# Performance work log

Hardware: AMD Instinct MI355X
Metric: run time of the kernel (lower is better)

## Reference

```python
import jax, jax.numpy as jnp
import numpy as np

INPUT_DIM = 29
OUTPUT_DIM = 67
ES = 256
HS = 512
SRC_LEN = 64
TRG_LEN = 48
BATCH = 512


def _lstm_cell(x, h, c, Wih, Whh, bih, bhh):
    # PyTorch gate order: i, f, g, o
    g = x @ Wih.T + bih + h @ Whh.T + bhh
    i, f, gg, o = jnp.split(g, 4, axis=-1)
    c_new = jax.nn.sigmoid(f) * c + jax.nn.sigmoid(i) * jnp.tanh(gg)
    h_new = jax.nn.sigmoid(o) * jnp.tanh(c_new)
    return h_new, c_new


def setup_inputs() -> dict:
    key = jax.random.key(0)
    ks = jax.random.split(key, 32)
    s_es = 1.0 / np.sqrt(ES)
    s_hs = 1.0 / np.sqrt(HS)
    inp = {}
    inp['src'] = jax.random.randint(ks[0], (SRC_LEN, BATCH), 0, INPUT_DIM)
    inp['trg'] = jax.random.randint(ks[1], (TRG_LEN, BATCH), 0, OUTPUT_DIM)
    # encoder params
    inp['enc_emb'] = jax.random.normal(ks[2], (INPUT_DIM, ES), jnp.float32)
    inp['enc_Wih_f'] = jax.random.normal(ks[3], (4 * HS, ES), jnp.float32) * s_hs
    inp['enc_Whh_f'] = jax.random.normal(ks[4], (4 * HS, HS), jnp.float32) * s_hs
    inp['enc_bih_f'] = jax.random.normal(ks[5], (4 * HS,), jnp.float32) * s_hs
    inp['enc_bhh_f'] = jax.random.normal(ks[6], (4 * HS,), jnp.float32) * s_hs
    inp['enc_Wih_b'] = jax.random.normal(ks[7], (4 * HS, ES), jnp.float32) * s_hs
    inp['enc_Whh_b'] = jax.random.normal(ks[8], (4 * HS, HS), jnp.float32) * s_hs
    inp['enc_bih_b'] = jax.random.normal(ks[9], (4 * HS,), jnp.float32) * s_hs
    inp['enc_bhh_b'] = jax.random.normal(ks[10], (4 * HS,), jnp.float32) * s_hs
    inp['fc_h_W'] = jax.random.normal(ks[11], (HS, 2 * HS), jnp.float32) * s_hs
    inp['fc_h_b'] = jax.random.normal(ks[12], (HS,), jnp.float32) * s_hs
    inp['fc_c_W'] = jax.random.normal(ks[13], (HS, 2 * HS), jnp.float32) * s_hs
    inp['fc_c_b'] = jax.random.normal(ks[14], (HS,), jnp.float32) * s_hs
    # decoder params
    inp['dec_emb'] = jax.random.normal(ks[15], (OUTPUT_DIM, ES), jnp.float32)
    inp['dec_Wih'] = jax.random.normal(ks[16], (4 * HS, 2 * HS + ES), jnp.float32) * s_hs
    inp['dec_Whh'] = jax.random.normal(ks[17], (4 * HS, HS), jnp.float32) * s_hs
    inp['dec_bih'] = jax.random.normal(ks[18], (4 * HS,), jnp.float32) * s_hs
    inp['dec_bhh'] = jax.random.normal(ks[19], (4 * HS,), jnp.float32) * s_hs
    inp['energy_W'] = jax.random.normal(ks[20], (1, 3 * HS), jnp.float32) * s_hs
    inp['energy_b'] = jax.random.normal(ks[21], (1,), jnp.float32) * s_hs
    inp['fc_out_W'] = jax.random.normal(ks[22], (OUTPUT_DIM, HS), jnp.float32) * s_hs
    inp['fc_out_b'] = jax.random.normal(ks[23], (OUTPUT_DIM,), jnp.float32) * s_hs
    return inp


def _forward(src, trg, enc_emb, enc_Wih_f, enc_Whh_f, enc_bih_f, enc_bhh_f,
             enc_Wih_b, enc_Whh_b, enc_bih_b, enc_bhh_b,
             fc_h_W, fc_h_b, fc_c_W, fc_c_b,
             dec_emb, dec_Wih, dec_Whh, dec_bih, dec_bhh,
             energy_W, energy_b, fc_out_W, fc_out_b):
    S, B = src.shape
    T = trg.shape[0]
    emb = enc_emb[src]  # [S, B, ES]
    h0 = jnp.zeros((B, HS), emb.dtype)
    c0 = jnp.zeros((B, HS), emb.dtype)

    def fwd_step(carry, x_t):
        h, c = carry
        h, c = _lstm_cell(x_t, h, c, enc_Wih_f, enc_Whh_f, enc_bih_f, enc_bhh_f)
        return (h, c), h

    def bwd_step(carry, x_t):
        h, c = carry
        h, c = _lstm_cell(x_t, h, c, enc_Wih_b, enc_Whh_b, enc_bih_b, enc_bhh_b)
        return (h, c), h

    (hf, cf), out_f = jax.lax.scan(fwd_step, (h0, c0), emb)
    (hb, cb), out_b_rev = jax.lax.scan(bwd_step, (h0, c0), emb[::-1])
    out_b = out_b_rev[::-1]
    encoder_states = jnp.concatenate([out_f, out_b], axis=2)  # [S, B, 2H]

    # fc_h / fc_c compress the 2 directions' final hidden/cell to [B, H]
    hidden_h = jnp.concatenate([hf, hb], axis=-1) @ fc_h_W.T + fc_h_b
    hidden_c = jnp.concatenate([cf, cb], axis=-1) @ fc_c_W.T + fc_c_b

    # Attention: original code passes encoder_hidden on EVERY step, so the
    # attention weights and context vector are constant across decode steps.
    h_rep = jnp.broadcast_to(hidden_h[None], (S, B, HS))
    e_in = jnp.concatenate([h_rep, encoder_states], axis=2)  # [S, B, 3H]
    energy = jax.nn.relu(e_in @ energy_W.T + energy_b)  # [S, B, 1]
    attn = jax.nn.softmax(energy, axis=0)[..., 0]  # [S, B]
    context = jnp.einsum('sb,sbh->bh', attn, encoder_states)  # [B, 2H]

    # Decode: teacher_forcing_ratio = 1.0 -> inputs are trg[t-1]; since the
    # rnn initial state is reset to encoder_hidden each step, all T-1 steps
    # are independent and can be computed in parallel.
    dec_in_tok = trg[:-1]  # [T-1, B]
    emb_d = dec_emb[dec_in_tok]  # [T-1, B, ES]
    ctx_rep = jnp.broadcast_to(context[None], (T - 1, B, 2 * HS))
    rnn_in = jnp.concatenate([ctx_rep, emb_d], axis=2)  # [T-1, B, 2H+ES]
    h_new, _ = _lstm_cell(rnn_in, hidden_h[None], hidden_c[None],
                          dec_Wih, dec_Whh, dec_bih, dec_bhh)
    logits = h_new @ fc_out_W.T + fc_out_b  # [T-1, B, V]
    outputs = jnp.concatenate(
        [jnp.zeros((1, B, OUTPUT_DIM), logits.dtype), logits], axis=0)
    return outputs


def reference(src, trg, enc_emb, enc_Wih_f, enc_Whh_f, enc_bih_f, enc_bhh_f,
              enc_Wih_b, enc_Whh_b, enc_bih_b, enc_bhh_b,
              fc_h_W, fc_h_b, fc_c_W, fc_c_b,
              dec_emb, dec_Wih, dec_Whh, dec_bih, dec_bhh,
              energy_W, energy_b, fc_out_W, fc_out_b):
    return _forward(src, trg, enc_emb, enc_Wih_f, enc_Whh_f, enc_bih_f,
                    enc_bhh_f, enc_Wih_b, enc_Whh_b, enc_bih_b, enc_bhh_b,
                    fc_h_W, fc_h_b, fc_c_W, fc_c_b, dec_emb, dec_Wih,
                    dec_Whh, dec_bih, dec_bhh, energy_W, energy_b,
                    fc_out_W, fc_out_b)
```

## Files before the change

kernel.cpp:

```cpp
#include <hip/hip_runtime.h>
#include <cstddef>

#define BATCH 512
#define ESZ   256
#define HSZ   512
#define G4    2048
#define SRCL  64
#define TRGL  48
#define ODIM  67

typedef __bf16  bf8v    __attribute__((ext_vector_type(8)));
typedef __bf16  bf4v    __attribute__((ext_vector_type(4)));
typedef float   floatx4 __attribute__((ext_vector_type(4)));

__device__ __forceinline__ floatx4 MF(bf8v a, bf8v b, floatx4 c) {
    return __builtin_amdgcn_mfma_f32_16x16x32_bf16(a, b, c, 0, 0, 0);
}

__device__ __forceinline__ float frcp(float x) { return __builtin_amdgcn_rcpf(x); }
__device__ __forceinline__ float fsig(float x) { return frcp(1.0f + __expf(-x)); }
__device__ __forceinline__ float ftanh(float x) { return 1.0f - 2.0f * frcp(1.0f + __expf(2.0f * x)); }

__device__ __forceinline__ bf8v cvt8(const float* __restrict__ s) {
    float4 a = *(const float4*)s;
    float4 b = *(const float4*)(s + 4);
    bf8v v;
    v[0] = (__bf16)a.x; v[1] = (__bf16)a.y; v[2] = (__bf16)a.z; v[3] = (__bf16)a.w;
    v[4] = (__bf16)b.x; v[5] = (__bf16)b.y; v[6] = (__bf16)b.z; v[7] = (__bf16)b.w;
    return v;
}

__global__ void embed_swz(const int* __restrict__ tok, const float* __restrict__ table,
                          __bf16* __restrict__ Az) {
    int i = blockIdx.x * 256 + threadIdx.x;
    int lane = i & 63;
    int kt = (i >> 6) & 7;
    int mt = (i >> 9) & 31;
    int t  = i >> 14;
    int b = mt * 16 + (lane & 15);
    int k = kt * 32 + (lane >> 4) * 8;
    int tk = tok[t * BATCH + b];
    (void)kt;
    *(bf8v*)(Az + (size_t)i * 8) = cvt8(table + (size_t)tk * ESZ + k);
}

__global__ void embdz(const int* __restrict__ trg, const float* __restrict__ table,
                      __bf16* __restrict__ Dz) {
    int i = blockIdx.x * 256 + threadIdx.x;
    int lane = i & 63;
    int kt = (i >> 6) & 7;
    int mt = i >> 9;
    int row = mt * 16 + (lane & 15);
    int k = kt * 32 + (lane >> 4) * 8;
    int tk = trg[row];
    *(bf8v*)(Dz + (size_t)i * 8) = cvt8(table + (size_t)tk * ESZ + k);
}

__global__ void zero_kernel(float* __restrict__ p, int n) {
    int i = blockIdx.x * 256 + threadIdx.x;
    if (i < n) p[i] = 0.f;
}

__global__ void bias_prep(const float* __restrict__ af, const float* __restrict__ bf,
                          const float* __restrict__ ab, const float* __restrict__ bb,
                          const float* __restrict__ ad, const float* __restrict__ bd,
                          float* __restrict__ of, float* __restrict__ ob, float* __restrict__ od) {
    int i = blockIdx.x * 256 + threadIdx.x;
    if (i < G4) { of[i] = af[i] + bf[i]; ob[i] = ab[i] + bb[i]; od[i] = ad[i] + bd[i]; }
}

__global__ void wswz_bf16(const float* __restrict__ Wih, const float* __restrict__ Whh,
                          __bf16* __restrict__ Wz) {
    int i = blockIdx.x * 256 + threadIdx.x;
    int lane = i & 63;
    int rest = i >> 6;
    int kt = rest % 24;
    int gj = rest / 24;
    int g = gj & 3, jt = gj >> 2;
    int row = g * 512 + jt * 16 + (lane & 15);
    int k = kt * 32 + (lane >> 4) * 8;
    const float* src = (k < ESZ) ? (Wih + (size_t)row * ESZ + k)
                                 : (Whh + (size_t)row * HSZ + (k - ESZ));
    *(bf8v*)(Wz + (size_t)i * 8) = cvt8(src);
}

__global__ void decwz(const float* __restrict__ dec_Wih, __bf16* __restrict__ Wz) {
    int i = blockIdx.x * 256 + threadIdx.x;
    int lane = i & 63;
    int kt = (i >> 6) & 7;
    int nt = i >> 9;
    int row = nt * 16 + (lane & 15);
    int k = kt * 32 + (lane >> 4) * 8;
    *(bf8v*)(Wz + (size_t)i * 8) =
        cvt8(dec_Wih + (size_t)row * (2 * HSZ + ESZ) + 2 * HSZ + k);
}

__global__ void wdcat_bf16(const float* __restrict__ dec_Wih, const float* __restrict__ dec_Whh,
                           __bf16* __restrict__ Wd) {
    int i = blockIdx.x * 256 + threadIdx.x;
    int n = i / 192;
    int e = (i - n * 192) << 3;
    const float* src = (e < 1024) ? (dec_Wih + (size_t)n * 1280 + e)
                                  : (dec_Whh + (size_t)n * HSZ + (e - 1024));
    *(bf8v*)(Wd + (size_t)n * 1536 + e) = cvt8(src);
}

__global__ void conv_f2b(const float* __restrict__ src, __bf16* __restrict__ dst, int n8) {
    int i = blockIdx.x * 256 + threadIdx.x;
    if (i < n8) *(bf8v*)(dst + (size_t)i * 8) = cvt8(src + (size_t)i * 8);
}

__global__ void fo_pad(const float* __restrict__ W, __bf16* __restrict__ dst) {
    int i = blockIdx.x * 256 + threadIdx.x;
    int r = i >> 6, e = (i & 63) << 3;
    bf8v v;
    if (r < ODIM) v = cvt8(W + (size_t)r * HSZ + e);
    else { for (int k = 0; k < 8; ++k) v[k] = (__bf16)0.f; }
    *(bf8v*)(dst + (size_t)r * HSZ + e) = v;
}

__global__ void fragswz(const __bf16* __restrict__ src, __bf16* __restrict__ dst,
                        int KT, int nchunks) {
    int i = blockIdx.x * 256 + threadIdx.x;
    if (i >= nchunks) return;
    int lane = i & 63;
    int kt = (i >> 6) % KT;
    int nt = (i >> 6) / KT;
    int row = nt * 16 + (lane & 15);
    int k = kt * 32 + (lane >> 4) * 8;
    *(bf8v*)(dst + (size_t)i * 8) = *(const bf8v*)(src + (size_t)row * (KT * 32) + k);
}

__global__ void cat_hfb(const __bf16* __restrict__ es, __bf16* __restrict__ dst) {
    int i = blockIdx.x * 256 + threadIdx.x;
    int r = i >> 7, e = (i & 127) << 3;
    const __bf16* s = (e < HSZ) ? (es + ((size_t)(63 * BATCH + r)) * 1024 + e)
                                : (es + (size_t)r * 1024 + e);
    *(bf8v*)(dst + (size_t)r * 1024 + e) = *(const bf8v*)s;
}

__global__ void cat_cfb(const float* __restrict__ cbuf, __bf16* __restrict__ dst) {
    int i = blockIdx.x * 256 + threadIdx.x;
    int r = i >> 7, e = (i & 127) << 3;
    const float* s = (e < HSZ) ? (cbuf + (size_t)r * HSZ + e)
                               : (cbuf + (size_t)BATCH * HSZ + (size_t)r * HSZ + (e - HSZ));
    *(bf8v*)(dst + (size_t)r * 1024 + e) = cvt8(s);
}

__global__ void cat_ctxh(const float* __restrict__ ctx, const float* __restrict__ hid_h,
                         __bf16* __restrict__ dst) {
    int i = blockIdx.x * 256 + threadIdx.x;
    int r = i / 192;
    int e = (i - r * 192) << 3;
    const float* s = (e < 1024) ? (ctx + (size_t)r * 1024 + e)
                                : (hid_h + (size_t)r * HSZ + (e - 1024));
    *(bf8v*)(dst + (size_t)r * 1536 + e) = cvt8(s);
}

__global__ void d0_swz(const float* __restrict__ D0, float* __restrict__ D0s) {
    int i = blockIdx.x * 256 + threadIdx.x;
    int b = i >> 11, rest = i & 2047, g = rest >> 9, j = rest & 511;
    D0s[(((size_t)b * 512 + j) << 2) + g] = D0[i];
}

__global__ __launch_bounds__(256) void enc_step6(
    const __bf16* __restrict__ Az, const __bf16* __restrict__ hPrev,
    __bf16* __restrict__ hNext, float* __restrict__ cbuf, __bf16* __restrict__ es,
    const __bf16* __restrict__ WzF, const __bf16* __restrict__ WzB,
    const float* __restrict__ biasF, const float* __restrict__ biasB, int t)
{
    __shared__ __bf16 Bh[4 * 16 * 64 * 8];
    __shared__ float  hT[64 * 17];

    const int dir = blockIdx.z;
    const int tt  = dir ? (SRCL - 1 - t) : t;
    const __bf16* Wz  = dir ? WzB : WzF;
    const float* bias = dir ? biasB : biasF;
    const int jt = blockIdx.x;
    const int j0 = jt * 16;
    const int m0 = blockIdx.y * 64;

    const int tid = threadIdx.x;
    const int w = tid >> 6, lane = tid & 63;
    const int quad = lane >> 4, l15 = lane & 15;

    const __bf16* WzJ = Wz + (((size_t)jt * 4 * 24) << 9);

#pragma unroll
    for (int it = 0; it < 16; ++it) {
        int idx = tid + it * 256;
        *(bf8v*)(Bh + ((size_t)idx << 3)) =
            *(const bf8v*)(WzJ + (((size_t)(((idx >> 10) * 24 + 8 + ((idx >> 6) & 15)) * 64
                                            + (idx & 63))) << 3));
    }

    const int mt = (m0 >> 4) + w;
    floatx4 acc[4] = {};

    const __bf16* ax = Az + ((((size_t)tt * 32 + mt) * 8) << 9) + lane * 8;
#pragma unroll
    for (int kt = 0; kt < 8; ++kt) {
        bf8v a = *(const bf8v*)(ax + ((size_t)kt << 9));
#pragma unroll
        for (int g = 0; g < 4; ++g) {
            bf8v b = *(const bf8v*)(WzJ + (((size_t)((g * 24 + kt) * 64 + lane)) << 3));
            acc[g] = MF(a, b, acc[g]);
        }
    }
    __syncthreads();
    const __bf16* ah = hPrev + ((((size_t)dir * 32 + mt) * 16) << 9) + lane * 8;
#pragma unroll 4
    for (int kt = 0; kt < 16; ++kt) {
        bf8v a = *(const bf8v*)(ah + ((size_t)kt << 9));
#pragma unroll
        for (int g = 0; g < 4; ++g) {
            bf8v b = *(const bf8v*)(Bh + (((size_t)((g * 16 + kt) * 64 + lane)) << 3));
            acc[g] = MF(a, b, acc[g]);
        }
    }

    const int j = j0 + l15;
    const float b0 = bias[j], b1 = bias[HSZ + j], b2 = bias[2 * HSZ + j], b3 = bias[3 * HSZ + j];
    const size_t cb = (size_t)dir * BATCH * HSZ;
    const int mwb = w * 16 + quad * 4;
#pragma unroll
    for (int r = 0; r < 4; ++r) {
        int m = m0 + mwb + r;
        float gi = acc[0][r] + b0;
        float gf = acc[1][r] + b1;
        float gg = acc[2][r] + b2;
        float go = acc[3][r] + b3;
        size_t ci = cb + (size_t)m * HSZ + j;
        float cn = fsig(gf) * cbuf[ci] + fsig(gi) * ftanh(gg);
        cbuf[ci] = cn;
        hT[(mwb + r) * 17 + l15] = fsig(go) * ftanh(cn);
    }
    __syncthreads();

    {
        int r = tid >> 2, ch = tid & 3;
        const float* hp = &hT[r * 17 + ch * 4];
        bf4v v;
#pragma unroll
        for (int e = 0; e < 4; ++e) v[e] = (__bf16)hp[e];
        *(bf4v*)(es + ((size_t)tt * BATCH + m0 + r) * 1024 + dir * HSZ + j0 + ch * 4) = v;
    }
    if (tid < 128) {
        int mtl = tid >> 5;
        int lnsub = tid & 31;
        int jhalf = (j0 >> 4) & 1;
        int ln = lnsub + jhalf * 32;
        int mloc = mtl * 16 + (lnsub & 15);
        int jloc = (lnsub >> 4) * 8;
        const float* hp = &hT[mloc * 17 + jloc];
        bf8v v;
#pragma unroll
        for (int e = 0; e < 8; ++e) v[e] = (__bf16)hp[e];
        size_t chunk = (((size_t)dir * 32 + (m0 >> 4) + mtl) * 16 + (j0 >> 5)) * 64 + ln;
        *(bf8v*)(hNext + chunk * 8) = v;
    }
}

__global__ __launch_bounds__(256) void dec_v6(
    const __bf16* __restrict__ Dz, const __bf16* __restrict__ Wz,
    const float* __restrict__ D0s, const float* __restrict__ hidc,
    __bf16* __restrict__ h_new)
{
    const int tid = threadIdx.x;
    const int w = tid >> 6, lane = tid & 63;
    const int quad = lane >> 4, l15 = lane & 15;
    const int jt = blockIdx.x;
    const int mt0 = blockIdx.y * 16 + w * 4;

    floatx4 acc[4][4] = {};
    const __bf16* az = Dz + (((size_t)mt0 * 8) << 9) + lane * 8;
#pragma unroll
    for (int kt = 0; kt < 8; ++kt) {
        bf8v a[4];
#pragma unroll
        for (int ms = 0; ms < 4; ++ms)
            a[ms] = *(const bf8v*)(az + (((size_t)(ms * 8 + kt)) << 9));
#pragma unroll
        for (int g = 0; g < 4; ++g) {
            bf8v b = *(const bf8v*)(Wz + (((size_t)(((g * 32 + jt) * 8 + kt) * 64 + lane)) << 3));
#pragma unroll
            for (int ms = 0; ms < 4; ++ms)
                acc[ms][g] = MF(a[ms], b, acc[ms][g]);
        }
    }
    const int j = jt * 16 + l15;
#pragma unroll
    for (int ms = 0; ms < 4; ++ms) {
        int mb = (mt0 + ms) * 16 + quad * 4;
#pragma unroll
        for (int r = 0; r < 4; ++r) {
            int m = mb + r;
            int b = m & (BATCH - 1);
            floatx4 d0 = *(const floatx4*)(D0s + (((size_t)b * 512 + j) << 2));
            float gi = acc[ms][0][r] + d0[0];
            float gf = acc[ms][1][r] + d0[1];
            float gg = acc[ms][2][r] + d0[2];
            float go = acc[ms][3][r] + d0[3];
            float cn = fsig(gf) * hidc[(size_t)b * HSZ + j] + fsig(gi) * ftanh(gg);
            h_new[(size_t)m * HSZ + j] = (__bf16)(fsig(go) * ftanh(cn));
        }
    }
}

__global__ __launch_bounds__(256) void gmmz(
    const __bf16* __restrict__ A, const __bf16* __restrict__ Bz, int K, int KT,
    const float* __restrict__ bias, float* __restrict__ C, int ldc, int N)
{
    const int tid = threadIdx.x;
    const int w = tid >> 6, lane = tid & 63;
    const int quad = lane >> 4, l15 = lane & 15;
    const int n0 = blockIdx.x * 64;
    const int mA = blockIdx.y * 64 + w * 16 + l15;
    const __bf16* Ar = A + (size_t)mA * K + quad * 8;

    floatx4 acc[4] = {};
    for (int kt = 0; kt < KT; ++kt) {
        bf8v a = *(const bf8v*)(Ar + kt * 32);
#pragma unroll
        for (int ns = 0; ns < 4; ++ns) {
            int jt = (n0 >> 4) + ns;
            bf8v b = *(const bf8v*)(Bz + (((size_t)((jt * KT + kt) * 64 + lane)) << 3));
            acc[ns] = MF(a, b, acc[ns]);
        }
    }
    const int mb = blockIdx.y * 64 + w * 16 + quad * 4;
#pragma unroll
    for (int ns = 0; ns < 4; ++ns) {
        int n = n0 + ns * 16 + l15;
        if (n < N) {
#pragma unroll
            for (int r = 0; r < 4; ++r)
                C[(size_t)(mb + r) * ldc + n] = acc[ns][r] + bias[n];
        }
    }
}

__global__ void eh_kernel(const float* __restrict__ hid_h, const float* __restrict__ eW,
                          const float* __restrict__ eb, float* __restrict__ eh) {
    int w = blockIdx.x * 4 + (threadIdx.x >> 6);
    int lane = threadIdx.x & 63;
    if (w >= BATCH) return;
    float s = 0.f;
    for (int k = lane; k < HSZ; k += 64) s += hid_h[(size_t)w * HSZ + k] * eW[k];
    for (int off = 32; off; off >>= 1) s += __shfl_down(s, off);
    if (lane == 0) eh[w] = s + eb[0];
}

__global__ void energy_kernel(const __bf16* __restrict__ es, const float* __restrict__ eW2,
                              const float* __restrict__ eh, float* __restrict__ energy) {
    int w = blockIdx.x * 4 + (threadIdx.x >> 6);
    int lane = threadIdx.x & 63;
    int s = w >> 9, b = w & 511;
    const __bf16* row = es + ((size_t)s * BATCH + b) * (2 * HSZ);
    float v = 0.f;
    for (int k = lane; k < 2 * HSZ; k += 64) v += (float)row[k] * eW2[k];
    for (int off = 32; off; off >>= 1) v += __shfl_down(v, off);
    if (lane == 0) energy[(size_t)s * BATCH + b] = fmaxf(v + eh[b], 0.f);
}

__global__ void softmax_kernel(const float* __restrict__ energy, float* __restrict__ attn) {
    int b = blockIdx.x * 4 + (threadIdx.x >> 6);
    int lane = threadIdx.x & 63;
    if (b >= BATCH) return;
    float v = energy[(size_t)lane * BATCH + b];
    float m = v;
    for (int off = 32; off; off >>= 1) m = fmaxf(m, __shfl_xor(m, off));
    float e = __expf(v - m);
    float sum = e;
    for (int off = 32; off; off >>= 1) sum += __shfl_xor(sum, off);
    attn[(size_t)lane * BATCH + b] = e / sum;
}

__global__ void context_kernel(const float* __restrict__ attn, const __bf16* __restrict__ es,
                               float* __restrict__ ctx) {
    int b = blockIdx.x;
    int j = threadIdx.x * 4;
    float a0 = 0.f, a1 = 0.f, a2 = 0.f, a3 = 0.f;
    for (int s = 0; s < SRCL; ++s) {
        float a = attn[(size_t)s * BATCH + b];
        const __bf16* r = es + ((size_t)s * BATCH + b) * (2 * HSZ) + j;
        a0 += a * (float)r[0]; a1 += a * (float)r[1];
        a2 += a * (float)r[2]; a3 += a * (float)r[3];
    }
    float4 o = make_float4(a0, a1, a2, a3);
    *(float4*)(ctx + (size_t)b * (2 * HSZ) + j) = o;
}

extern "C" void kernel_launch(void* const* d_in, const int* in_sizes, int n_in,
                              void* d_out, int out_size, void* d_ws, size_t ws_size,
                              hipStream_t stream) {
    const int*   src      = (const int*)d_in[0];
    const int*   trg      = (const int*)d_in[1];
    const float* enc_emb  = (const float*)d_in[2];
    const float* Wih_f    = (const float*)d_in[3];
    const float* Whh_f    = (const float*)d_in[4];
    const float* bih_f    = (const float*)d_in[5];
    const float* bhh_f    = (const float*)d_in[6];
    const float* Wih_b    = (const float*)d_in[7];
    const float* Whh_b    = (const float*)d_in[8];
    const float* bih_b    = (const float*)d_in[9];
    const float* bhh_b    = (const float*)d_in[10];
    const float* fc_h_W   = (const float*)d_in[11];
    const float* fc_h_b   = (const float*)d_in[12];
    const float* fc_c_W   = (const float*)d_in[13];
    const float* fc_c_b   = (const float*)d_in[14];
    const float* dec_emb  = (const float*)d_in[15];
    const float* dec_Wih  = (const float*)d_in[16];
    const float* dec_Whh  = (const float*)d_in[17];
    const float* dec_bih  = (const float*)d_in[18];
    const float* dec_bhh  = (const float*)d_in[19];
    const float* energy_W = (const float*)d_in[20];
    const float* energy_b = (const float*)d_in[21];
    const float* fc_out_W = (const float*)d_in[22];
    const float* fc_out_b = (const float*)d_in[23];
    float* out = (float*)d_out;

    float* ws = (float*)d_ws;
    size_t o = 0;
    __bf16* Az   = (__bf16*)(ws + o); o += 4194304;
    __bf16* Dz   = (__bf16*)(ws + o); o += 3080192;
    __bf16* es   = (__bf16*)(ws + o); o += 16777216;
    float* zbase = ws + o;
    __bf16* h0   = (__bf16*)(ws + o); o += 262144;
    __bf16* h1   = (__bf16*)(ws + o); o += 262144;
    float*  cbuf = ws + o;            o += 524288;
    __bf16* WzF  = (__bf16*)(ws + o); o += 786432;
    __bf16* WzB  = (__bf16*)(ws + o); o += 786432;
    __bf16* decWzp=(__bf16*)(ws + o); o += 262144;
    __bf16* WdC  = (__bf16*)(ws + o); o += 1572864;
    __bf16* WdZ  = (__bf16*)(ws + o); o += 1572864;
    __bf16* fcWh = (__bf16*)(ws + o); o += 262144;
    __bf16* fcWhZ= (__bf16*)(ws + o); o += 262144;
    __bf16* fcWc = (__bf16*)(ws + o); o += 262144;
    __bf16* fcWcZ= (__bf16*)(ws + o); o += 262144;
    __bf16* foWb = (__bf16*)(ws + o); o += 32768;
    __bf16* foWz = (__bf16*)(ws + o); o += 32768;
    __bf16* hfb  = (__bf16*)(ws + o); o += 262144;
    __bf16* cfb  = (__bf16*)(ws + o); o += 262144;
    __bf16* ctxh = (__bf16*)(ws + o); o += 393216;
    float* hid_h = ws + o;            o += 262144;
    float* hid_c = ws + o;            o += 262144;
    float* ehv   = ws + o;            o += 512;
    float* energy= ws + o;            o += 32768;
    float* attn  = ws + o;            o += 32768;
    float* ctx   = ws + o;            o += 524288;
    float* D0    = ws + o;            o += 1048576;
    float* D0s   = ws + o;            o += 1048576;
    float* bias_f= ws + o;            o += 2048;
    float* bias_b= ws + o;            o += 2048;
    float* bias_d= ws + o;            o += 2048;
    __bf16* h_new= (__bf16*)(ws + o); o += 6160384;

    embed_swz<<<4096, 256, 0, stream>>>(src, enc_emb, Az);
    embdz<<<3008, 256, 0, stream>>>(trg, dec_emb, Dz);
    zero_kernel<<<4096, 256, 0, stream>>>(zbase, 1048576);
    bias_prep<<<8, 256, 0, stream>>>(bih_f, bhh_f, bih_b, bhh_b, dec_bih, dec_bhh,
                                     bias_f, bias_b, bias_d);
    wswz_bf16<<<768, 256, 0, stream>>>(Wih_f, Whh_f, WzF);
    wswz_bf16<<<768, 256, 0, stream>>>(Wih_b, Whh_b, WzB);
    decwz<<<256, 256, 0, stream>>>(dec_Wih, decWzp);
    wdcat_bf16<<<1536, 256, 0, stream>>>(dec_Wih, dec_Whh, WdC);
    fragswz<<<1536, 256, 0, stream>>>(WdC, WdZ, 48, 393216);
    conv_f2b<<<256, 256, 0, stream>>>(fc_h_W, fcWh, 65536);
    fragswz<<<256, 256, 0, stream>>>(fcWh, fcWhZ, 32, 65536);
    conv_f2b<<<256, 256, 0, stream>>>(fc_c_W, fcWc, 65536);
    fragswz<<<256, 256, 0, stream>>>(fcWc, fcWcZ, 32, 65536);
    fo_pad<<<32, 256, 0, stream>>>(fc_out_W, foWb);
    fragswz<<<32, 256, 0, stream>>>(foWb, foWz, 16, 8192);

    for (int t = 0; t < SRCL; ++t) {
        const __bf16* hp = (t & 1) ? h1 : h0;
        __bf16*       hn = (t & 1) ? h0 : h1;
        enc_step6<<<dim3(32, 8, 2), 256, 0, stream>>>(
            Az, hp, hn, cbuf, es, WzF, WzB, bias_f, bias_b, t);
    }

    cat_hfb<<<256, 256, 0, stream>>>(es, hfb);
    cat_cfb<<<256, 256, 0, stream>>>(cbuf, cfb);
    gmmz<<<dim3(8, 8), 256, 0, stream>>>(hfb, fcWhZ, 1024, 32, fc_h_b, hid_h, HSZ, HSZ);
    gmmz<<<dim3(8, 8), 256, 0, stream>>>(cfb, fcWcZ, 1024, 32, fc_c_b, hid_c, HSZ, HSZ);

    eh_kernel<<<128, 256, 0, stream>>>(hid_h, energy_W, energy_b, ehv);
    energy_kernel<<<8192, 256, 0, stream>>>(es, energy_W + HSZ, ehv, energy);
    softmax_kernel<<<128, 256, 0, stream>>>(energy, attn);
    context_kernel<<<512, 256, 0, stream>>>(attn, es, ctx);

    cat_ctxh<<<384, 256, 0, stream>>>(ctx, hid_h, ctxh);
    gmmz<<<dim3(32, 8), 256, 0, stream>>>(ctxh, WdZ, 1536, 48, bias_d, D0, G4, G4);
    d0_swz<<<4096, 256, 0, stream>>>(D0, D0s);

    dec_v6<<<dim3(32, 94), 256, 0, stream>>>(Dz, decWzp, D0s, hid_c, h_new);

    zero_kernel<<<134, 256, 0, stream>>>(out, BATCH * ODIM);
    gmmz<<<dim3(2, 376), 256, 0, stream>>>(h_new, foWz, HSZ, 16, fc_out_b,
                                           out + (size_t)BATCH * ODIM, ODIM, ODIM);
}
```

Measured before the change: 1.163 ms.

## Fuse the encoder time loop into one persistent scan kernel

Replaces the 64 per-timestep encoder launches with one persistent kernel. Each of 64 blocks owns 16 batch rows of one direction and covers all hidden units, so the recurrent state h stays in LDS (double-buffered) and c stays in registers for the whole sequence. This removes the per-step launch overhead, the global h ping-pong buffers and their zeroing kernel. In exchange only 64 workgroups run, and each one streams its direction's full weight matrix from L2 or memory on every step instead of caching a slice in LDS, so the recurrence may become bandwidth- and latency-bound.

```diff
diff --git a/kernel.cpp b/kernel.cpp
--- a/kernel.cpp
+++ b/kernel.cpp
@@ -34,13 +34,11 @@
                           __bf16* __restrict__ Az) {
     int i = blockIdx.x * 256 + threadIdx.x;
     int lane = i & 63;
-    int kt = (i >> 6) & 7;
     int mt = (i >> 9) & 31;
     int t  = i >> 14;
     int b = mt * 16 + (lane & 15);
-    int k = kt * 32 + (lane >> 4) * 8;
+    int k = ((i >> 6) & 7) * 32 + (lane >> 4) * 8;
     int tk = tok[t * BATCH + b];
-    (void)kt;
     *(bf8v*)(Az + (size_t)i * 8) = cvt8(table + (size_t)tk * ESZ + k);
 }
 
@@ -163,102 +161,103 @@
     D0s[(((size_t)b * 512 + j) << 2) + g] = D0[i];
 }
 
-__global__ __launch_bounds__(256) void enc_step6(
-    const __bf16* __restrict__ Az, const __bf16* __restrict__ hPrev,
-    __bf16* __restrict__ hNext, float* __restrict__ cbuf, __bf16* __restrict__ es,
+__global__ __launch_bounds__(1024) void enc_scan2(
+    const __bf16* __restrict__ Az,
+    float* __restrict__ cbuf, __bf16* __restrict__ es,
     const __bf16* __restrict__ WzF, const __bf16* __restrict__ WzB,
-    const float* __restrict__ biasF, const float* __restrict__ biasB, int t)
+    const float* __restrict__ biasF, const float* __restrict__ biasB)
 {
-    __shared__ __bf16 Bh[4 * 16 * 64 * 8];
-    __shared__ float  hT[64 * 17];
-
-    const int dir = blockIdx.z;
-    const int tt  = dir ? (SRCL - 1 - t) : t;
-    const __bf16* Wz  = dir ? WzB : WzF;
-    const float* bias = dir ? biasB : biasF;
-    const int jt = blockIdx.x;
-    const int j0 = jt * 16;
-    const int m0 = blockIdx.y * 64;
+    __shared__ __bf16 hbuf[2][16 * 512];
+
+    const int bid = blockIdx.x;
+    const int dir = (bid & 7) >> 2;
+    const int mt  = (bid >> 3) * 4 + (bid & 3);
+    const int m0  = mt * 16;
+
+    const __bf16* Wz   = dir ? WzB : WzF;
+    const float*  bias = dir ? biasB : biasF;
 
     const int tid = threadIdx.x;
     const int w = tid >> 6, lane = tid & 63;
     const int quad = lane >> 4, l15 = lane & 15;
 
-    const __bf16* WzJ = Wz + (((size_t)jt * 4 * 24) << 9);
-
-#pragma unroll
-    for (int it = 0; it < 16; ++it) {
-        int idx = tid + it * 256;
-        *(bf8v*)(Bh + ((size_t)idx << 3)) =
-            *(const bf8v*)(WzJ + (((size_t)(((idx >> 10) * 24 + 8 + ((idx >> 6) & 15)) * 64
-                                            + (idx & 63))) << 3));
-    }
-
-    const int mt = (m0 >> 4) + w;
-    floatx4 acc[4] = {};
-
-    const __bf16* ax = Az + ((((size_t)tt * 32 + mt) * 8) << 9) + lane * 8;
-#pragma unroll
-    for (int kt = 0; kt < 8; ++kt) {
-        bf8v a = *(const bf8v*)(ax + ((size_t)kt << 9));
-#pragma unroll
-        for (int g = 0; g < 4; ++g) {
-            bf8v b = *(const bf8v*)(WzJ + (((size_t)((g * 24 + kt) * 64 + lane)) << 3));
-            acc[g] = MF(a, b, acc[g]);
-        }
-    }
+    {
+        bf8v z = {};
+        *(bf8v*)(&hbuf[0][tid * 8]) = z;
+    }
+
+    float bsv[2][4];
+    int jj[2];
+#pragma unroll
+    for (int jth = 0; jth < 2; ++jth) {
+        jj[jth] = (2 * w + jth) * 16 + l15;
+#pragma unroll
+        for (int g = 0; g < 4; ++g) bsv[jth][g] = bias[g * HSZ + jj[jth]];
+    }
+    const __bf16* wzb = Wz + (size_t)(w * 192) * 512 + lane * 8;
+
+    float creg[2][4] = {};
     __syncthreads();
-    const __bf16* ah = hPrev + ((((size_t)dir * 32 + mt) * 16) << 9) + lane * 8;
+
+    for (int t = 0; t < SRCL; ++t) {
+        const int tt = dir ? (SRCL - 1 - t) : t;
+        const int cur = t & 1;
+        floatx4 acc[2][4] = {};
+
+        const __bf16* axb = Az + (((size_t)tt * 32 + mt) * 8) * 512 + lane * 8;
+#pragma unroll
+        for (int kt = 0; kt < 8; ++kt) {
+            bf8v a = *(const bf8v*)(axb + kt * 512);
+#pragma unroll
+            for (int jth = 0; jth < 2; ++jth)
+#pragma unroll
+                for (int g = 0; g < 4; ++g) {
+                    bf8v b = *(const bf8v*)(wzb + (size_t)((jth * 4 + g) * 24 + kt) * 512);
+                    acc[jth][g] = MF(a, b, acc[jth][g]);
+                }
+        }
+        const __bf16* ahb = &hbuf[cur][lane * 8];
 #pragma unroll 4
-    for (int kt = 0; kt < 16; ++kt) {
-        bf8v a = *(const bf8v*)(ah + ((size_t)kt << 9));
-#pragma unroll
-        for (int g = 0; g < 4; ++g) {
-            bf8v b = *(const bf8v*)(Bh + (((size_t)((g * 16 + kt) * 64 + lane)) << 3));
-            acc[g] = MF(a, b, acc[g]);
-        }
-    }
-
-    const int j = j0 + l15;
-    const float b0 = bias[j], b1 = bias[HSZ + j], b2 = bias[2 * HSZ + j], b3 = bias[3 * HSZ + j];
-    const size_t cb = (size_t)dir * BATCH * HSZ;
-    const int mwb = w * 16 + quad * 4;
-#pragma unroll
-    for (int r = 0; r < 4; ++r) {
-        int m = m0 + mwb + r;
-        float gi = acc[0][r] + b0;
-        float gf = acc[1][r] + b1;
-        float gg = acc[2][r] + b2;
-        float go = acc[3][r] + b3;
-        size_t ci = cb + (size_t)m * HSZ + j;
-        float cn = fsig(gf) * cbuf[ci] + fsig(gi) * ftanh(gg);
-        cbuf[ci] = cn;
-        hT[(mwb + r) * 17 + l15] = fsig(go) * ftanh(cn);
-    }
-    __syncthreads();
-
-    {
-        int r = tid >> 2, ch = tid & 3;
-        const float* hp = &hT[r * 17 + ch * 4];
-        bf4v v;
-#pragma unroll
-        for (int e = 0; e < 4; ++e) v[e] = (__bf16)hp[e];
-        *(bf4v*)(es + ((size_t)tt * BATCH + m0 + r) * 1024 + dir * HSZ + j0 + ch * 4) = v;
-    }
-    if (tid < 128) {
-        int mtl = tid >> 5;
-        int lnsub = tid & 31;
-        int jhalf = (j0 >> 4) & 1;
-        int ln = lnsub + jhalf * 32;
-        int mloc = mtl * 16 + (lnsub & 15);
-        int jloc = (lnsub >> 4) * 8;
-        const float* hp = &hT[mloc * 17 + jloc];
-        bf8v v;
-#pragma unroll
-        for (int e = 0; e < 8; ++e) v[e] = (__bf16)hp[e];
-        size_t chunk = (((size_t)dir * 32 + (m0 >> 4) + mtl) * 16 + (j0 >> 5)) * 64 + ln;
-        *(bf8v*)(hNext + chunk * 8) = v;
-    }
+        for (int kt = 0; kt < 16; ++kt) {
+            bf8v a = *(const bf8v*)(ahb + kt * 512);
+#pragma unroll
+            for (int jth = 0; jth < 2; ++jth)
+#pragma unroll
+                for (int g = 0; g < 4; ++g) {
+                    bf8v b = *(const bf8v*)(wzb + (size_t)((jth * 4 + g) * 24 + 8 + kt) * 512);
+                    acc[jth][g] = MF(a, b, acc[jth][g]);
+                }
+        }
+
+        __bf16* hn = &hbuf[cur ^ 1][0];
+        const size_t esrow = ((size_t)tt * BATCH + m0) * 1024 + (size_t)dir * HSZ;
+#pragma unroll
+        for (int jth = 0; jth < 2; ++jth) {
+            const int j = jj[jth];
+            const int koff = (j >> 5) * 512 + ((j >> 3) & 3) * 128 + (j & 7);
+#pragma unroll
+            for (int r = 0; r < 4; ++r) {
+                const int m = quad * 4 + r;
+                float gi = acc[jth][0][r] + bsv[jth][0];
+                float gf = acc[jth][1][r] + bsv[jth][1];
+                float gg = acc[jth][2][r] + bsv[jth][2];
+                float go = acc[jth][3][r] + bsv[jth][3];
+                float cn = fsig(gf) * creg[jth][r] + fsig(gi) * ftanh(gg);
+                creg[jth][r] = cn;
+                float hv = fsig(go) * ftanh(cn);
+                hn[koff + m * 8] = (__bf16)hv;
+                es[esrow + (size_t)m * 1024 + j] = (__bf16)hv;
+            }
+        }
+        __syncthreads();
+    }
+
+#pragma unroll
+    for (int jth = 0; jth < 2; ++jth)
+#pragma unroll
+        for (int r = 0; r < 4; ++r)
+            cbuf[(size_t)dir * BATCH * HSZ + (size_t)(m0 + quad * 4 + r) * HSZ + jj[jth]]
+                = creg[jth][r];
 }
 
 __global__ __launch_bounds__(256) void dec_v6(
@@ -425,9 +424,6 @@
     __bf16* Az   = (__bf16*)(ws + o); o += 4194304;
     __bf16* Dz   = (__bf16*)(ws + o); o += 3080192;
     __bf16* es   = (__bf16*)(ws + o); o += 16777216;
-    float* zbase = ws + o;
-    __bf16* h0   = (__bf16*)(ws + o); o += 262144;
-    __bf16* h1   = (__bf16*)(ws + o); o += 262144;
     float*  cbuf = ws + o;            o += 524288;
     __bf16* WzF  = (__bf16*)(ws + o); o += 786432;
     __bf16* WzB  = (__bf16*)(ws + o); o += 786432;
@@ -458,7 +454,6 @@
 
     embed_swz<<<4096, 256, 0, stream>>>(src, enc_emb, Az);
     embdz<<<3008, 256, 0, stream>>>(trg, dec_emb, Dz);
-    zero_kernel<<<4096, 256, 0, stream>>>(zbase, 1048576);
     bias_prep<<<8, 256, 0, stream>>>(bih_f, bhh_f, bih_b, bhh_b, dec_bih, dec_bhh,
                                      bias_f, bias_b, bias_d);
     wswz_bf16<<<768, 256, 0, stream>>>(Wih_f, Whh_f, WzF);
@@ -473,12 +468,7 @@
     fo_pad<<<32, 256, 0, stream>>>(fc_out_W, foWb);
     fragswz<<<32, 256, 0, stream>>>(foWb, foWz, 16, 8192);
 
-    for (int t = 0; t < SRCL; ++t) {
-        const __bf16* hp = (t & 1) ? h1 : h0;
-        __bf16*       hn = (t & 1) ? h0 : h1;
-        enc_step6<<<dim3(32, 8, 2), 256, 0, stream>>>(
-            Az, hp, hn, cbuf, es, WzF, WzB, bias_f, bias_b, t);
-    }
+    enc_scan2<<<64, 1024, 0, stream>>>(Az, cbuf, es, WzF, WzB, bias_f, bias_b);
 
     cat_hfb<<<256, 256, 0, stream>>>(es, hfb);
     cat_cfb<<<256, 256, 0, stream>>>(cbuf, cfb);
```

Measured after the change: 4.047 ms. 3.48x slower.
